# Optimization experiments

Hardware: AMD Instinct MI355X
Metric: run time of the kernel (lower is better)

Reference implementation:

```python
import jax, jax.numpy as jnp
from jax import lax
import numpy as np

N, L, LQ, D, AF, K = 4096, 512, 32, 30, 10, 4  # n_sents, sent_len, q_len, embed_dim, extra feats, conv size


def setup_inputs() -> dict:
    key = jax.random.key(0)
    ks = jax.random.split(key, 10)
    fan_conv = 1.0 / np.sqrt(D * K)
    fan_lin = 1.0 / np.sqrt(AF + 3)
    return {
        "sents_embeds": jax.random.normal(ks[0], (N, L, D), jnp.float32),
        "question_embeds": jax.random.normal(ks[1], (LQ, D), jnp.float32),
        "sents_gaf": jax.random.normal(ks[2], (N, AF), jnp.float32),
        "sents_labels": jax.random.randint(ks[3], (N,), 0, 2),
        "conv1_w": jax.random.uniform(ks[4], (D, D, K), jnp.float32, -fan_conv, fan_conv),
        "conv1_b": jax.random.uniform(ks[5], (D,), jnp.float32, -fan_conv, fan_conv),
        "conv2_w": jax.random.uniform(ks[6], (D, D, K), jnp.float32, -fan_conv, fan_conv),
        "conv2_b": jax.random.uniform(ks[7], (D,), jnp.float32, -fan_conv, fan_conv),
        "lin_w": jax.random.uniform(ks[8], (2, AF + 3), jnp.float32, -fan_lin, fan_lin),
        "lin_b": jax.random.uniform(ks[9], (2,), jnp.float32, -fan_lin, fan_lin),
    }


def _conv1d(x, w, b):
    # x: [B, C, T], w: [O, I, K] (torch layout), padding = K-1 both sides (as torch padding=K-1)
    y = lax.conv_general_dilated(x, w, window_strides=(1,), padding=[(K - 1, K - 1)],
                                 dimension_numbers=("NCW", "OIW", "NCW"))
    return y + b[None, :, None]


def _window_pool(x):
    # avg_pool1d(kernel=K, stride=1) over last axis
    return lax.reduce_window(x, 0.0, lax.add, (1, 1, K), (1, 1, 1), "VALID") / K


def _gpool(x):
    # global average pool over last axis -> [B, C]
    return jnp.mean(x, axis=-1)


def _cos(a, b):
    # a: [N, D] or [D], b: [N, D] or [D] -> cosine similarity, broadcasting
    num = jnp.sum(a * b, axis=-1)
    den = jnp.linalg.norm(a, axis=-1) * jnp.linalg.norm(b, axis=-1)
    return num / den


def _forward(sents_embeds, question_embeds, sents_gaf, sents_labels,
             conv1_w, conv1_b, conv2_w, conv2_b, lin_w, lin_b):
    q = question_embeds.T[None]                # [1, D, LQ]
    s = jnp.transpose(sents_embeds, (0, 2, 1))  # [N, D, L]

    # question side (identical every loop iteration in the original)
    q_raw = _gpool(q)[0]                        # [D]
    q1c = _conv1d(q, conv1_w, conv1_b)          # [1, D, LQ+3]
    q1g = _gpool(q1c)[0]                        # [D]
    q1w = _window_pool(q1c)                     # [1, D, LQ]
    q2c = _conv1d(q1w, conv2_w, conv2_b)        # [1, D, LQ+3]
    q2g = _gpool(q2c)[0]                        # [D]

    # sentence side, batched over N
    s_raw = _gpool(s)                           # [N, D]
    s1c = _conv1d(s, conv1_w, conv1_b)          # [N, D, L+3]
    s1g = _gpool(s1c)                           # [N, D]
    s1w = _window_pool(s1c)                     # [N, D, L]
    s2c = _conv1d(s1w, conv2_w, conv2_b)        # [N, D, L+3]
    s2g = _gpool(s2c)                           # [N, D]

    # sim1: original overwrites quest_global_pool in the loop, so i=0 uses the raw
    # question pool and i>0 use the conv2-level question pool from the prior iter.
    sim1_raw = _cos(q_raw[None], s_raw)         # [N]
    sim1_q2 = _cos(q2g[None], s_raw)            # [N]
    sim1 = jnp.where(jnp.arange(s_raw.shape[0]) == 0, sim1_raw, sim1_q2)
    sim2 = _cos(q1g[None], s1g)                 # [N]
    sim3 = _cos(q2g[None], s2g)                 # [N]

    mlp_in = jnp.concatenate([sim1[:, None], sim2[:, None], sim3[:, None], sents_gaf], axis=-1)  # [N, 13]
    logits = mlp_in @ lin_w.T + lin_b           # [N, 2]
    logp = jax.nn.log_softmax(logits, axis=-1)
    cost = -jnp.mean(jnp.take_along_axis(logp, sents_labels[:, None], axis=-1)[:, 0])
    emit = jax.nn.softmax(logp, axis=-1)[:, 1]  # softmax applied to log_softmax, as in original
    return cost, emit


def reference(sents_embeds, question_embeds, sents_gaf, sents_labels,
              conv1_w, conv1_b, conv2_w, conv2_b, lin_w, lin_b):
    return _forward(sents_embeds, question_embeds, sents_gaf, sents_labels,
                    conv1_w, conv1_b, conv2_w, conv2_b, lin_w, lin_b)
```

## Files before the change

### kernel.cpp

```cpp
#include <hip/hip_runtime.h>
#include <math.h>

#define NS 4096
#define LL 512
#define LQS 32
#define DD 30
#define AFN 10
#define KW 4

enum {
  QRAW = 0,
  Q1G  = 30,
  Q2G  = 60,
  NRM  = 90,
  WS1  = 96,
  WS2  = 996,
  OA0  = 1896,
  OA1  = 2796,
  OA2  = 3696,
  OB0  = 4596,
  OB1  = 5496,
  OB2  = 6396,
  WS_TOTAL = 7296
};

__global__ __launch_bounds__(256) void prep_kernel(
    const float* __restrict__ qe,
    const float* __restrict__ w1,
    const float* __restrict__ b1,
    const float* __restrict__ w2,
    const float* __restrict__ b2,
    float* __restrict__ ws,
    float* __restrict__ out)
{
    __shared__ float qT[DD][LQS];
    __shared__ float q1c[DD][LQS + 3];
    __shared__ float q1w[DD][LQS];
    __shared__ float q2c[DD][LQS + 3];
    __shared__ float qpool[3][DD];
    const int tid = threadIdx.x;

    for (int f = tid; f < LQS * DD; f += 256) {
        qT[f % DD][f / DD] = qe[f];
    }
    __syncthreads();

    for (int idx = tid; idx < DD * (LQS + 3); idx += 256) {
        int o = idx / (LQS + 3), t = idx % (LQS + 3);
        float acc = b1[o];
        for (int i = 0; i < DD; i++) {
            const float* w = w1 + (o * DD + i) * KW;
            #pragma unroll
            for (int k = 0; k < KW; k++) {
                int j = t + k - 3;
                if (j >= 0 && j < LQS) acc += qT[i][j] * w[k];
            }
        }
        q1c[o][t] = acc;
    }
    __syncthreads();

    for (int idx = tid; idx < DD * LQS; idx += 256) {
        int o = idx / LQS, t = idx % LQS;
        q1w[o][t] = 0.25f * (q1c[o][t] + q1c[o][t + 1] + q1c[o][t + 2] + q1c[o][t + 3]);
    }
    __syncthreads();

    for (int idx = tid; idx < DD * (LQS + 3); idx += 256) {
        int o = idx / (LQS + 3), t = idx % (LQS + 3);
        float acc = b2[o];
        for (int i = 0; i < DD; i++) {
            const float* w = w2 + (o * DD + i) * KW;
            #pragma unroll
            for (int k = 0; k < KW; k++) {
                int j = t + k - 3;
                if (j >= 0 && j < LQS) acc += q1w[i][j] * w[k];
            }
        }
        q2c[o][t] = acc;
    }
    __syncthreads();

    if (tid < DD) {
        float a = 0.f;
        for (int t = 0; t < LQS; t++) a += qT[tid][t];
        qpool[0][tid] = a * (1.0f / LQS);
        float g1 = 0.f;
        for (int t = 0; t < LQS + 3; t++) g1 += q1c[tid][t];
        qpool[1][tid] = g1 * (1.0f / (LQS + 3));
        float g2 = 0.f;
        for (int t = 0; t < LQS + 3; t++) g2 += q2c[tid][t];
        qpool[2][tid] = g2 * (1.0f / (LQS + 3));
        ws[QRAW + tid] = qpool[0][tid];
        ws[Q1G + tid]  = qpool[1][tid];
        ws[Q2G + tid]  = qpool[2][tid];
    }
    __syncthreads();
    if (tid < 3) {
        float s = 0.f;
        for (int i = 0; i < DD; i++) { float v = qpool[tid][i]; s += v * v; }
        ws[NRM + tid] = sqrtf(s);
    }
    if (tid == 0) out[0] = 0.0f;

    for (int idx = tid; idx < DD * DD; idx += 256) {
        const float* w = w1 + idx * KW;
        float a = w[0], b = w[1], c = w[2], d = w[3];
        ws[WS1 + idx] = a + b + c + d;
        ws[OA0 + idx] = 3.f * d + 2.f * c + b;
        ws[OA1 + idx] = 2.f * d + c;
        ws[OA2 + idx] = d;
        ws[OB0 + idx] = a;
        ws[OB1 + idx] = b + 2.f * a;
        ws[OB2 + idx] = c + 2.f * b + 3.f * a;
        const float* v = w2 + idx * KW;
        ws[WS2 + idx] = v[0] + v[1] + v[2] + v[3];
    }
}

__global__ __launch_bounds__(256) void sent_kernel(
    const float* __restrict__ se,
    const float* __restrict__ gaf,
    const int*   __restrict__ labels,
    const float* __restrict__ b1,
    const float* __restrict__ b2,
    const float* __restrict__ linw,
    const float* __restrict__ linb,
    const float* __restrict__ ws,
    float* __restrict__ out)
{
    const int n = blockIdx.x;
    const int tid = threadIdx.x;
    const float* base = se + (size_t)n * (LL * DD);

    __shared__ float partial[960];
    __shared__ float bnd[6][DD];
    __shared__ float S[DD], Tv[DD], s1g[DD], s2g[DD];
    __shared__ float red[6][32];

    if (tid < 240) {
        const float4* p = (const float4*)base + tid;
        float4 acc = make_float4(0.f, 0.f, 0.f, 0.f);
        #pragma unroll
        for (int it = 0; it < 16; it++) {
            float4 v = p[it * 240];
            acc.x += v.x; acc.y += v.y; acc.z += v.z; acc.w += v.w;
        }
        partial[4 * tid + 0] = acc.x;
        partial[4 * tid + 1] = acc.y;
        partial[4 * tid + 2] = acc.z;
        partial[4 * tid + 3] = acc.w;
    }
    if (tid < 180) {
        int r = tid / DD, c = tid % DD;
        int j = (r < 3) ? r : (LL - 6 + r);
        bnd[r][c] = base[j * DD + c];
    }
    __syncthreads();

    if (tid < DD) {
        float a = 0.f;
        #pragma unroll
        for (int m = 0; m < 32; m++) a += partial[tid + DD * m];
        S[tid] = a;
    }
    __syncthreads();

    if (tid < DD) {
        const int i = tid;
        const float* ws1 = ws + WS1 + i * DD;
        const float* a0  = ws + OA0 + i * DD;
        const float* a1  = ws + OA1 + i * DD;
        const float* a2  = ws + OA2 + i * DD;
        const float* c0  = ws + OB0 + i * DD;
        const float* c1  = ws + OB1 + i * DD;
        const float* c2  = ws + OB2 + i * DD;
        float dotS = 0.f, edge = 0.f;
        for (int ii = 0; ii < DD; ii++) {
            dotS += S[ii] * ws1[ii];
            edge += bnd[0][ii] * a0[ii] + bnd[1][ii] * a1[ii] + bnd[2][ii] * a2[ii]
                  + bnd[3][ii] * c0[ii] + bnd[4][ii] * c1[ii] + bnd[5][ii] * c2[ii];
        }
        const float bias = b1[i];
        s1g[i] = dotS * (1.0f / (LL + 3)) + bias;
        Tv[i]  = dotS + (float)LL * bias - 0.25f * edge;
    }
    __syncthreads();

    if (tid < DD) {
        const float* ws2 = ws + WS2 + tid * DD;
        float a = 0.f;
        for (int ii = 0; ii < DD; ii++) a += Tv[ii] * ws2[ii];
        s2g[tid] = a * (1.0f / (LL + 3)) + b2[tid];
    }
    __syncthreads();

    if (tid < DD) {
        float qv = (n == 0) ? ws[QRAW + tid] : ws[Q2G + tid];
        red[0][tid] = qv * S[tid];
        red[1][tid] = S[tid] * S[tid];
        red[2][tid] = ws[Q1G + tid] * s1g[tid];
        red[3][tid] = s1g[tid] * s1g[tid];
        red[4][tid] = ws[Q2G + tid] * s2g[tid];
        red[5][tid] = s2g[tid] * s2g[tid];
    }
    __syncthreads();
    if (tid < 6) {
        float a = 0.f;
        for (int i = 0; i < DD; i++) a += red[tid][i];
        red[tid][31] = a;
    }
    __syncthreads();

    if (tid == 0) {
        float nq = (n == 0) ? ws[NRM + 0] : ws[NRM + 2];
        float sim1 = red[0][31] / (nq * sqrtf(red[1][31]));
        float sim2 = red[2][31] / (ws[NRM + 1] * sqrtf(red[3][31]));
        float sim3 = red[4][31] / (ws[NRM + 2] * sqrtf(red[5][31]));

        float in[3 + AFN];
        in[0] = sim1; in[1] = sim2; in[2] = sim3;
        const float* g = gaf + (size_t)n * AFN;
        #pragma unroll
        for (int j = 0; j < AFN; j++) in[3 + j] = g[j];

        float l0 = linb[0], l1 = linb[1];
        #pragma unroll
        for (int j = 0; j < 3 + AFN; j++) {
            l0 += in[j] * linw[j];
            l1 += in[j] * linw[(3 + AFN) + j];
        }
        float m = fmaxf(l0, l1);
        float lse = m + logf(expf(l0 - m) + expf(l1 - m));
        float lp0 = l0 - lse, lp1 = l1 - lse;
        float mm = fmaxf(lp0, lp1);
        float e0 = expf(lp0 - mm), e1 = expf(lp1 - mm);
        out[1 + n] = e1 / (e0 + e1);
        int lab = labels[n];
        float lp = (lab == 0) ? lp0 : lp1;
        atomicAdd(&out[0], -lp * (1.0f / NS));
    }
}

extern "C" void kernel_launch(void* const* d_in, const int* in_sizes, int n_in,
                              void* d_out, int out_size, void* d_ws, size_t ws_size,
                              hipStream_t stream)
{
    (void)in_sizes; (void)n_in; (void)out_size; (void)ws_size;
    const float* se  = (const float*)d_in[0];
    const float* qe  = (const float*)d_in[1];
    const float* gaf = (const float*)d_in[2];
    const int*   lab = (const int*)d_in[3];
    const float* w1  = (const float*)d_in[4];
    const float* b1  = (const float*)d_in[5];
    const float* w2  = (const float*)d_in[6];
    const float* b2  = (const float*)d_in[7];
    const float* lw  = (const float*)d_in[8];
    const float* lb  = (const float*)d_in[9];
    float* out = (float*)d_out;
    float* ws  = (float*)d_ws;

    hipLaunchKernelGGL(prep_kernel, dim3(1), dim3(256), 0, stream,
                       qe, w1, b1, w2, b2, ws, out);
    hipLaunchKernelGGL(sent_kernel, dim3(NS), dim3(256), 0, stream,
                       se, gaf, lab, b1, b2, lw, lb, ws, out);
}
```

Measured before the change: 493.4 us.

## Split sentence kernel into streaming reduction and wave-per-sentence post kernel

```diff
diff --git a/kernel.cpp b/kernel.cpp
--- a/kernel.cpp
+++ b/kernel.cpp
@@ -21,7 +21,8 @@
   OB0  = 4596,
   OB1  = 5496,
   OB2  = 6396,
-  WS_TOTAL = 7296
+  SARR = 7296,
+  WS_TOTAL = SARR + NS * DD
 };
 
 __global__ __launch_bounds__(256) void prep_kernel(
@@ -118,7 +119,40 @@
     }
 }
 
-__global__ __launch_bounds__(256) void sent_kernel(
+__global__ __launch_bounds__(256) void stream_kernel(
+    const float* __restrict__ se,
+    float* __restrict__ ws)
+{
+    const int n = blockIdx.x;
+    const int tid = threadIdx.x;
+    const float* base = se + (size_t)n * (LL * DD);
+
+    __shared__ float partial[960];
+
+    if (tid < 240) {
+        const float4* p = (const float4*)base + tid;
+        float sx = 0.f, sy = 0.f, sz = 0.f, sw = 0.f;
+        #pragma unroll
+        for (int it = 0; it < 16; it++) {
+            float4 v = p[it * 240];
+            sx += v.x; sy += v.y; sz += v.z; sw += v.w;
+        }
+        partial[4 * tid + 0] = sx;
+        partial[4 * tid + 1] = sy;
+        partial[4 * tid + 2] = sz;
+        partial[4 * tid + 3] = sw;
+    }
+    __syncthreads();
+
+    if (tid < DD) {
+        float a = 0.f;
+        #pragma unroll
+        for (int m = 0; m < 32; m++) a += partial[tid + DD * m];
+        ws[SARR + n * DD + tid] = a;
+    }
+}
+
+__global__ __launch_bounds__(256) void post_kernel(
     const float* __restrict__ se,
     const float* __restrict__ gaf,
     const int*   __restrict__ labels,
@@ -129,94 +163,88 @@
     const float* __restrict__ ws,
     float* __restrict__ out)
 {
-    const int n = blockIdx.x;
-    const int tid = threadIdx.x;
-    const float* base = se + (size_t)n * (LL * DD);
-
-    __shared__ float partial[960];
-    __shared__ float bnd[6][DD];
-    __shared__ float S[DD], Tv[DD], s1g[DD], s2g[DD];
-    __shared__ float red[6][32];
-
-    if (tid < 240) {
-        const float4* p = (const float4*)base + tid;
-        float4 acc = make_float4(0.f, 0.f, 0.f, 0.f);
-        #pragma unroll
-        for (int it = 0; it < 16; it++) {
-            float4 v = p[it * 240];
-            acc.x += v.x; acc.y += v.y; acc.z += v.z; acc.w += v.w;
-        }
-        partial[4 * tid + 0] = acc.x;
-        partial[4 * tid + 1] = acc.y;
-        partial[4 * tid + 2] = acc.z;
-        partial[4 * tid + 3] = acc.w;
-    }
-    if (tid < 180) {
-        int r = tid / DD, c = tid % DD;
-        int j = (r < 3) ? r : (LL - 6 + r);
-        bnd[r][c] = base[j * DD + c];
-    }
-    __syncthreads();
-
-    if (tid < DD) {
-        float a = 0.f;
-        #pragma unroll
-        for (int m = 0; m < 32; m++) a += partial[tid + DD * m];
-        S[tid] = a;
-    }
-    __syncthreads();
-
-    if (tid < DD) {
-        const int i = tid;
-        const float* ws1 = ws + WS1 + i * DD;
-        const float* a0  = ws + OA0 + i * DD;
-        const float* a1  = ws + OA1 + i * DD;
-        const float* a2  = ws + OA2 + i * DD;
-        const float* c0  = ws + OB0 + i * DD;
-        const float* c1  = ws + OB1 + i * DD;
-        const float* c2  = ws + OB2 + i * DD;
-        float dotS = 0.f, edge = 0.f;
-        for (int ii = 0; ii < DD; ii++) {
-            dotS += S[ii] * ws1[ii];
-            edge += bnd[0][ii] * a0[ii] + bnd[1][ii] * a1[ii] + bnd[2][ii] * a2[ii]
-                  + bnd[3][ii] * c0[ii] + bnd[4][ii] * c1[ii] + bnd[5][ii] * c2[ii];
-        }
-        const float bias = b1[i];
-        s1g[i] = dotS * (1.0f / (LL + 3)) + bias;
-        Tv[i]  = dotS + (float)LL * bias - 0.25f * edge;
-    }
-    __syncthreads();
-
-    if (tid < DD) {
-        const float* ws2 = ws + WS2 + tid * DD;
-        float a = 0.f;
-        for (int ii = 0; ii < DD; ii++) a += Tv[ii] * ws2[ii];
-        s2g[tid] = a * (1.0f / (LL + 3)) + b2[tid];
-    }
-    __syncthreads();
-
-    if (tid < DD) {
-        float qv = (n == 0) ? ws[QRAW + tid] : ws[Q2G + tid];
-        red[0][tid] = qv * S[tid];
-        red[1][tid] = S[tid] * S[tid];
-        red[2][tid] = ws[Q1G + tid] * s1g[tid];
-        red[3][tid] = s1g[tid] * s1g[tid];
-        red[4][tid] = ws[Q2G + tid] * s2g[tid];
-        red[5][tid] = s2g[tid] * s2g[tid];
-    }
-    __syncthreads();
-    if (tid < 6) {
-        float a = 0.f;
-        for (int i = 0; i < DD; i++) a += red[tid][i];
-        red[tid][31] = a;
-    }
-    __syncthreads();
-
-    if (tid == 0) {
+    const int tid  = threadIdx.x;
+    const int wid  = tid >> 6;
+    const int lane = tid & 63;
+    const int n    = blockIdx.x * 4 + wid;
+
+    __shared__ float costp[4];
+
+    const bool act = (lane < DD);
+    const int  ic  = act ? lane : 0;
+
+    float S_i = 0.f, e0r = 0.f, e1r = 0.f, e2r = 0.f, e3r = 0.f, e4r = 0.f, e5r = 0.f;
+    float bb1, bb2;
+    {
+        const float* base = se + (size_t)n * (LL * DD);
+        S_i = ws[SARR + n * DD + ic];
+        e0r = base[0 * DD + ic];
+        e1r = base[1 * DD + ic];
+        e2r = base[2 * DD + ic];
+        e3r = base[509 * DD + ic];
+        e4r = base[510 * DD + ic];
+        e5r = base[511 * DD + ic];
+        bb1 = b1[ic];
+        bb2 = b2[ic];
+    }
+
+    float dotS = 0.f, edge = 0.f;
+    const float* ws1 = ws + WS1 + ic * DD;
+    const float* a0  = ws + OA0 + ic * DD;
+    const float* a1  = ws + OA1 + ic * DD;
+    const float* a2  = ws + OA2 + ic * DD;
+    const float* c0  = ws + OB0 + ic * DD;
+    const float* c1  = ws + OB1 + ic * DD;
+    const float* c2  = ws + OB2 + ic * DD;
+    #pragma unroll 6
+    for (int ii = 0; ii < DD; ii++) {
+        float s  = __shfl(S_i, ii, 64);
+        float b0 = __shfl(e0r, ii, 64);
+        float b1v = __shfl(e1r, ii, 64);
+        float b2v = __shfl(e2r, ii, 64);
+        float b3v = __shfl(e3r, ii, 64);
+        float b4v = __shfl(e4r, ii, 64);
+        float b5v = __shfl(e5r, ii, 64);
+        dotS += s * ws1[ii];
+        edge += b0 * a0[ii] + b1v * a1[ii] + b2v * a2[ii]
+              + b3v * c0[ii] + b4v * c1[ii] + b5v * c2[ii];
+    }
+    float s1g = dotS * (1.0f / (LL + 3)) + bb1;
+    float Tv  = dotS + (float)LL * bb1 - 0.25f * edge;
+
+    float dot2 = 0.f;
+    const float* ws2 = ws + WS2 + ic * DD;
+    #pragma unroll 6
+    for (int ii = 0; ii < DD; ii++) {
+        float tv = __shfl(Tv, ii, 64);
+        dot2 += tv * ws2[ii];
+    }
+    float s2g = dot2 * (1.0f / (LL + 3)) + bb2;
+
+    float qv = (n == 0) ? ws[QRAW + ic] : ws[Q2G + ic];
+    float q1 = ws[Q1G + ic];
+    float q2 = ws[Q2G + ic];
+    float p0 = act ? qv * S_i : 0.f;
+    float p1 = act ? S_i * S_i : 0.f;
+    float p2 = act ? q1 * s1g : 0.f;
+    float p3 = act ? s1g * s1g : 0.f;
+    float p4 = act ? q2 * s2g : 0.f;
+    float p5 = act ? s2g * s2g : 0.f;
+    #pragma unroll
+    for (int off = 32; off >= 1; off >>= 1) {
+        p0 += __shfl_xor(p0, off, 64);
+        p1 += __shfl_xor(p1, off, 64);
+        p2 += __shfl_xor(p2, off, 64);
+        p3 += __shfl_xor(p3, off, 64);
+        p4 += __shfl_xor(p4, off, 64);
+        p5 += __shfl_xor(p5, off, 64);
+    }
+
+    if (lane == 0) {
         float nq = (n == 0) ? ws[NRM + 0] : ws[NRM + 2];
-        float sim1 = red[0][31] / (nq * sqrtf(red[1][31]));
-        float sim2 = red[2][31] / (ws[NRM + 1] * sqrtf(red[3][31]));
-        float sim3 = red[4][31] / (ws[NRM + 2] * sqrtf(red[5][31]));
+        float sim1 = p0 / (nq * sqrtf(p1));
+        float sim2 = p2 / (ws[NRM + 1] * sqrtf(p3));
+        float sim3 = p4 / (ws[NRM + 2] * sqrtf(p5));
 
         float in[3 + AFN];
         in[0] = sim1; in[1] = sim2; in[2] = sim3;
@@ -234,11 +262,15 @@
         float lse = m + logf(expf(l0 - m) + expf(l1 - m));
         float lp0 = l0 - lse, lp1 = l1 - lse;
         float mm = fmaxf(lp0, lp1);
-        float e0 = expf(lp0 - mm), e1 = expf(lp1 - mm);
-        out[1 + n] = e1 / (e0 + e1);
+        float ee0 = expf(lp0 - mm), ee1 = expf(lp1 - mm);
+        out[1 + n] = ee1 / (ee0 + ee1);
         int lab = labels[n];
         float lp = (lab == 0) ? lp0 : lp1;
-        atomicAdd(&out[0], -lp * (1.0f / NS));
+        costp[wid] = -lp * (1.0f / NS);
+    }
+    __syncthreads();
+    if (tid == 0) {
+        atomicAdd(&out[0], costp[0] + costp[1] + costp[2] + costp[3]);
     }
 }
 
@@ -262,6 +294,8 @@
 
     hipLaunchKernelGGL(prep_kernel, dim3(1), dim3(256), 0, stream,
                        qe, w1, b1, w2, b2, ws, out);
-    hipLaunchKernelGGL(sent_kernel, dim3(NS), dim3(256), 0, stream,
+    hipLaunchKernelGGL(stream_kernel, dim3(NS), dim3(256), 0, stream,
+                       se, ws);
+    hipLaunchKernelGGL(post_kernel, dim3(NS / 4), dim3(256), 0, stream,
                        se, gaf, lab, b1, b2, lw, lb, ws, out);
 }
```

After: 489.6 us. Within noise of the previous version (-0.8%).
